# Performance work log

Measured on AMD Instinct MI355X. Metric: run time of the kernel, lower is better.

Reference implementation:

```python
import jax, jax.numpy as jnp
import numpy as np
from jax import lax

D_MODEL = 64      # feature_dim
D_STATE = 16      # state_dim
D_CONV = 4        # conv_dim
EXPAND = 2
D_INNER = EXPAND * D_MODEL          # 128
DT_RANK = (D_MODEL + 15) // 16      # ceil(d_model/16) = 4, mamba default
IN_DIM = 64
LN_EPS = 1e-3                        # keras LayerNormalization default epsilon


def setup_inputs() -> dict:
    key = jax.random.key(0)
    ks = jax.random.split(key, 12)
    B, L = 16, 8192
    s = 0.02
    x = jax.random.normal(ks[0], (B, L, IN_DIM), jnp.float32)
    W_in = jax.random.normal(ks[1], (IN_DIM, D_MODEL), jnp.float32) * s
    b_in = jnp.zeros((D_MODEL,), jnp.float32)
    in_proj_w = jax.random.normal(ks[2], (D_MODEL, 2 * D_INNER), jnp.float32) * s
    conv_w = jax.random.normal(ks[3], (D_INNER, D_CONV), jnp.float32) * 0.1
    conv_b = jnp.zeros((D_INNER,), jnp.float32)
    x_proj_w = jax.random.normal(ks[4], (D_INNER, DT_RANK + 2 * D_STATE), jnp.float32) * s
    dt_proj_w = jax.random.normal(ks[5], (DT_RANK, D_INNER), jnp.float32) * (DT_RANK ** -0.5)
    # dt bias init so softplus(dt) lands roughly in [dt_min, dt_max]
    dt = jnp.exp(jax.random.uniform(ks[6], (D_INNER,)) * (np.log(0.1) - np.log(0.001)) + np.log(0.001))
    dt_proj_b = dt + jnp.log(-jnp.expm1(-dt))  # inverse softplus
    A_log = jnp.log(jnp.broadcast_to(jnp.arange(1, D_STATE + 1, dtype=jnp.float32), (D_INNER, D_STATE)))
    D_skip = jnp.ones((D_INNER,), jnp.float32)
    out_proj_w = jax.random.normal(ks[7], (D_INNER, D_MODEL), jnp.float32) * s
    ln_gamma = jnp.ones((D_MODEL,), jnp.float32)
    ln_beta = jnp.zeros((D_MODEL,), jnp.float32)
    return {"x": x, "W_in": W_in, "b_in": b_in, "in_proj_w": in_proj_w,
            "conv_w": conv_w, "conv_b": conv_b, "x_proj_w": x_proj_w,
            "dt_proj_w": dt_proj_w, "dt_proj_b": dt_proj_b, "A_log": A_log,
            "D_skip": D_skip, "out_proj_w": out_proj_w,
            "ln_gamma": ln_gamma, "ln_beta": ln_beta}


def reference(x, W_in, b_in, in_proj_w, conv_w, conv_b, x_proj_w,
              dt_proj_w, dt_proj_b, A_log, D_skip, out_proj_w, ln_gamma, ln_beta):
    B, L, _ = x.shape
    # Conv1D kernel_size=1 input projection
    xin = x @ W_in + b_in                          # [B,L,D_MODEL]
    # --- Mamba ---
    xz = xin @ in_proj_w                           # [B,L,2*D_INNER]
    xc, z = xz[..., :D_INNER], xz[..., D_INNER:]
    # causal depthwise conv (groups=d_inner, padding=d_conv-1, crop to L)
    xp = jnp.pad(xc, ((0, 0), (D_CONV - 1, 0), (0, 0)))
    xconv = conv_b
    for k in range(D_CONV):
        xconv = xconv + xp[:, k:k + L, :] * conv_w[:, k]
    u = jax.nn.silu(xconv)                         # [B,L,D_INNER]
    dbc = u @ x_proj_w                             # [B,L,DT_RANK+2*D_STATE]
    dt = jax.nn.softplus(dbc[..., :DT_RANK] @ dt_proj_w + dt_proj_b)   # [B,L,D_INNER]
    Bm = dbc[..., DT_RANK:DT_RANK + D_STATE]       # [B,L,D_STATE]
    Cm = dbc[..., DT_RANK + D_STATE:]              # [B,L,D_STATE]
    A = -jnp.exp(A_log)                            # [D_INNER,D_STATE]

    def step(h, xs):
        dt_t, b_t, c_t, u_t = xs                   # [B,Di],[B,Ds],[B,Ds],[B,Di]
        dA = jnp.exp(dt_t[:, :, None] * A)         # [B,Di,Ds]
        h = dA * h + (dt_t * u_t)[:, :, None] * b_t[:, None, :]
        y = jnp.einsum('bds,bs->bd', h, c_t)
        return h, y

    xs = (jnp.swapaxes(dt, 0, 1), jnp.swapaxes(Bm, 0, 1),
          jnp.swapaxes(Cm, 0, 1), jnp.swapaxes(u, 0, 1))
    h0 = jnp.zeros((B, D_INNER, D_STATE), x.dtype)
    _, ys = lax.scan(step, h0, xs)                 # ys: [L,B,D_INNER]
    y = jnp.swapaxes(ys, 0, 1) + u * D_skip
    y = y * jax.nn.silu(z)
    h_out = y @ out_proj_w                         # [B,L,D_MODEL]
    # residual + LayerNorm
    res = h_out + xin
    mu = jnp.mean(res, axis=-1, keepdims=True)
    var = jnp.mean(jnp.square(res - mu), axis=-1, keepdims=True)
    return ln_gamma * (res - mu) * lax.rsqrt(var + LN_EPS) + ln_beta
```

## Files before the change

### kernel.cpp

```cpp
#include <hip/hip_runtime.h>
#include <hip/hip_bf16.h>
#include <hip/hip_fp16.h>

#define B_SZ   16
#define L_SZ   8192
#define DM     64
#define DI     128
#define NCH    256
#define CLEN   32
#define CH     64
#define RT     80
#define PA     72
#define PU     136
#define PC     132
#define LN_EPS 1e-3f

typedef float  f4 __attribute__((ext_vector_type(4)));
typedef short  s8 __attribute__((ext_vector_type(8)));
typedef unsigned short u16;
typedef unsigned int   u32;
#define MFMA16 __builtin_amdgcn_mfma_f32_16x16x32_bf16

__device__ __forceinline__ u16 f2bfu(float f) {
    u32 u = __float_as_uint(f);
    return (u16)((u + 0x7FFFu + ((u >> 16) & 1u)) >> 16);
}
__device__ __forceinline__ u32 pk2bf(float a, float b) {
    return (u32)f2bfu(a) | ((u32)f2bfu(b) << 16);
}
__device__ __forceinline__ float bflo(u32 u) { return __uint_as_float(u << 16); }
__device__ __forceinline__ float bfhi(u32 u) { return __uint_as_float(u & 0xFFFF0000u); }
__device__ __forceinline__ float bfu2f(u16 h) { return __uint_as_float((u32)h << 16); }
__device__ __forceinline__ float h2f(u32 lo16) {
    return __half2float(__ushort_as_half((u16)(lo16 & 0xFFFFu)));
}
__device__ __forceinline__ float fsig(float v) {
    return __builtin_amdgcn_rcpf(1.f + __expf(-v));
}
__device__ __forceinline__ float fsp(float v) {
    return fmaxf(v, 0.f) + __logf(1.f + __expf(-fabsf(v)));
}

__global__ __launch_bounds__(256) void k_prep(
    const float* __restrict__ W_in, const float* __restrict__ in_proj,
    const float* __restrict__ x_proj, const float* __restrict__ Wout,
    u16* __restrict__ Wf1, u16* __restrict__ Wf2,
    u16* __restrict__ Wf3, u16* __restrict__ Wf4)
{
    const int tid = threadIdx.x;
    for (int g = tid; g < 512; g += 256) {
        int lane = g & 63, ks = (g >> 6) & 1, nt = g >> 7;
        int n = nt * 16 + (lane & 15), kb = ks * 32 + (lane >> 4) * 8;
        for (int j = 0; j < 8; j++) Wf1[g * 8 + j] = f2bfu(W_in[(kb + j) * 64 + n]);
    }
    for (int g = tid; g < 2048; g += 256) {
        int lane = g & 63, ks = (g >> 6) & 1, nt = g >> 7;
        int n = nt * 16 + (lane & 15), kb = ks * 32 + (lane >> 4) * 8;
        for (int j = 0; j < 8; j++) Wf2[g * 8 + j] = f2bfu(in_proj[(kb + j) * 256 + n]);
    }
    for (int g = tid; g < 768; g += 256) {
        int lane = g & 63, ks = (g >> 6) & 3, nt = g >> 8;
        int n = nt * 16 + (lane & 15), kb = ks * 32 + (lane >> 4) * 8;
        for (int j = 0; j < 8; j++)
            Wf3[g * 8 + j] = f2bfu(n < 36 ? x_proj[(kb + j) * 36 + n] : 0.f);
    }
    for (int g = tid; g < 1024; g += 256) {
        int lane = g & 63, ks = (g >> 6) & 3, nt = g >> 8;
        int n = nt * 16 + (lane & 15), kb = ks * 32 + (lane >> 4) * 8;
        for (int j = 0; j < 8; j++) Wf4[g * 8 + j] = f2bfu(Wout[(kb + j) * 64 + n]);
    }
}

__global__ __launch_bounds__(256, 4) void k_frontend(
    const float* __restrict__ x, const float* __restrict__ b_in,
    const float* __restrict__ conv_w, const float* __restrict__ conv_b,
    const float* __restrict__ dt_w, const float* __restrict__ dt_b,
    const u16* __restrict__ Wf1, const u16* __restrict__ Wf2, const u16* __restrict__ Wf3,
    const float* __restrict__ A_log,
    float* __restrict__ xin_g, u32* __restrict__ dtu_g,
    float* __restrict__ B_g, float* __restrict__ C_g, u16* __restrict__ sz_g,
    float* __restrict__ hl_ws, float* __restrict__ sdt_ws)
{
    __shared__ __align__(16) char sm[40736];
    u16*   smA   = (u16*)sm;
    u16*   smB   = (u16*)(sm + 11520);
    u16*   smU   = (u16*)sm;
    float* smDtr = (float*)(sm + 17408);
    float* smBf  = (float*)(sm + 18432);
    u16*   smC   = (u16*)(sm + 23040);
    u32*   smDt  = (u32*)(sm + 23040);

    const int tid = threadIdx.x;
    const int w = tid >> 6, lane = tid & 63;
    const int n16 = lane & 15, quad = lane >> 4;
    const int b = blockIdx.y, c0 = blockIdx.x * CH;
    const long long tokbase = (long long)b * L_SZ + c0;

    for (int idx = tid; idx < RT * 16; idx += 256) {
        int r = idx >> 4, c4 = idx & 15;
        int l = c0 - 3 + r;
        float4 v = make_float4(0.f, 0.f, 0.f, 0.f);
        if (r < 67 && l >= 0)
            v = *(const float4*)(x + ((long long)b * L_SZ + l) * 64 + c4 * 4);
        *(uint2*)((char*)smA + r * 144 + c4 * 8) = make_uint2(pk2bf(v.x, v.y), pk2bf(v.z, v.w));
    }
    __syncthreads();

    {
        s8 b0 = *(const s8*)(Wf1 + ((w * 2 + 0) * 64 + lane) * 8);
        s8 b1 = *(const s8*)(Wf1 + ((w * 2 + 1) * 64 + lane) * 8);
        float bias = b_in[w * 16 + n16];
        for (int m = 0; m < 5; m++) {
            int ar = m * 16 + n16;
            s8 a0 = *(const s8*)(smA + ar * PA + quad * 8);
            s8 a1 = *(const s8*)(smA + ar * PA + 32 + quad * 8);
            f4 acc = {0.f, 0.f, 0.f, 0.f};
            acc = MFMA16(a0, b0, acc, 0, 0, 0);
            acc = MFMA16(a1, b1, acc, 0, 0, 0);
#pragma unroll
            for (int reg = 0; reg < 4; reg++) {
                int rr = m * 16 + quad * 4 + reg;
                float v = acc[reg] + bias;
                smB[rr * PA + w * 16 + n16] = f2bfu(v);
                if (rr >= 3 && rr < 67)
                    xin_g[(tokbase + rr - 3) * 64 + w * 16 + n16] = v;
            }
        }
    }
    __syncthreads();

    {
        s8 bf[4][2];
#pragma unroll
        for (int i = 0; i < 4; i++)
#pragma unroll
            for (int ks = 0; ks < 2; ks++)
                bf[i][ks] = *(const s8*)(Wf2 + (((w * 4 + i) * 2 + ks) * 64 + lane) * 8);
        for (int m = 0; m < 5; m++) {
            int ar = m * 16 + n16;
            s8 a0 = *(const s8*)(smB + ar * PA + quad * 8);
            s8 a1 = *(const s8*)(smB + ar * PA + 32 + quad * 8);
#pragma unroll
            for (int i = 0; i < 4; i++) {
                f4 acc = {0.f, 0.f, 0.f, 0.f};
                acc = MFMA16(a0, bf[i][0], acc, 0, 0, 0);
                acc = MFMA16(a1, bf[i][1], acc, 0, 0, 0);
                int cg = (w * 4 + i) * 16 + n16;
#pragma unroll
                for (int reg = 0; reg < 4; reg++) {
                    int rr = m * 16 + quad * 4 + reg;
                    float v = acc[reg];
                    if (cg < 128) {
                        if (rr < 67) {
                            int l = c0 - 3 + rr;
                            smC[rr * PC + cg] = f2bfu(l >= 0 ? v : 0.f);
                        }
                    } else if (rr >= 3 && rr < 67) {
                        sz_g[(tokbase + rr - 3) * 128 + (cg - 128)] = f2bfu(v * fsig(v));
                    }
                }
            }
        }
    }
    __syncthreads();

    {
        const int d2 = lane * 2, ctb = w * 16;
        float4 cw0 = ((const float4*)conv_w)[d2];
        float4 cw1 = ((const float4*)conv_w)[d2 + 1];
        float cb0 = conv_b[d2], cb1 = conv_b[d2 + 1];
        u32 r0 = *(const u32*)((char*)smC + (ctb + 0) * 264 + lane * 4);
        u32 r1 = *(const u32*)((char*)smC + (ctb + 1) * 264 + lane * 4);
        u32 r2 = *(const u32*)((char*)smC + (ctb + 2) * 264 + lane * 4);
#pragma unroll 4
        for (int j = 0; j < 16; j++) {
            int ct = ctb + j;
            u32 r3 = *(const u32*)((char*)smC + (ct + 3) * 264 + lane * 4);
            float v0 = cb0 + bflo(r0) * cw0.x + bflo(r1) * cw0.y + bflo(r2) * cw0.z + bflo(r3) * cw0.w;
            float v1 = cb1 + bfhi(r0) * cw1.x + bfhi(r1) * cw1.y + bfhi(r2) * cw1.z + bfhi(r3) * cw1.w;
            u32 pk = pk2bf(v0 * fsig(v0), v1 * fsig(v1));
            *(u32*)(smU + ct * PU + d2) = pk;
            r0 = r1; r1 = r2; r2 = r3;
        }
    }
    __syncthreads();

    {
        s8 bf3[3][4];
#pragma unroll
        for (int nt = 0; nt < 3; nt++)
#pragma unroll
            for (int ks = 0; ks < 4; ks++)
                bf3[nt][ks] = *(const s8*)(Wf3 + ((nt * 4 + ks) * 64 + lane) * 8);
        f4 acc[3] = {{0.f,0.f,0.f,0.f},{0.f,0.f,0.f,0.f},{0.f,0.f,0.f,0.f}};
        int ar = w * 16 + n16;
#pragma unroll
        for (int ks = 0; ks < 4; ks++) {
            s8 a = *(const s8*)(smU + ar * PU + ks * 32 + quad * 8);
#pragma unroll
            for (int nt = 0; nt < 3; nt++) acc[nt] = MFMA16(a, bf3[nt][ks], acc[nt], 0, 0, 0);
        }
#pragma unroll
        for (int nt = 0; nt < 3; nt++) {
            int c = nt * 16 + n16;
#pragma unroll
            for (int reg = 0; reg < 4; reg++) {
                int rr = w * 16 + quad * 4 + reg;
                float v = acc[nt][reg];
                long long t = tokbase + rr;
                if (c < 4)       smDtr[rr * 4 + c] = v;
                else if (c < 20) { B_g[t * 16 + (c - 4)] = v; smBf[rr * 16 + (c - 4)] = v; }
                else if (c < 36) C_g[t * 16 + (c - 20)] = v;
            }
        }
    }
    __syncthreads();

    {
        const int o2 = lane * 2, grp = w;
        float w00 = dt_w[o2],       w01 = dt_w[o2 + 1];
        float w10 = dt_w[128 + o2], w11 = dt_w[128 + o2 + 1];
        float w20 = dt_w[256 + o2], w21 = dt_w[256 + o2 + 1];
        float w30 = dt_w[384 + o2], w31 = dt_w[384 + o2 + 1];
        float b0 = dt_b[o2], b1 = dt_b[o2 + 1];
#pragma unroll 4
        for (int j = 0; j < 16; j++) {
            int ct = grp * 16 + j;
            float4 q = *(const float4*)(smDtr + ct * 4);
            float v0 = b0 + q.x * w00 + q.y * w10 + q.z * w20 + q.w * w30;
            float v1 = b1 + q.x * w01 + q.y * w11 + q.z * w21 + q.w * w31;
            u32 hpk = (u32)__half_as_ushort(__float2half_rn(fsp(v0))) |
                      ((u32)__half_as_ushort(__float2half_rn(fsp(v1))) << 16);
            smDt[ct * 64 + lane] = hpk;
            u32 upk = *(const u32*)(smU + ct * PU + o2);
            u32 pk0 = (hpk & 0xFFFFu) | (upk << 16);
            u32 pk1 = (hpk >> 16) | (upk & 0xFFFF0000u);
            *(uint2*)(dtu_g + (tokbase + ct) * 128 + o2) = make_uint2(pk0, pk1);
        }
    }
    __syncthreads();

    {
        const int d = tid & 127, cs = tid >> 7;
        const int j2 = d >> 1, hi = d & 1;
        float A[16];
#pragma unroll
        for (int s = 0; s < 16; s++) A[s] = -__expf(A_log[d * 16 + s]);
        const float A0 = A[0];
        bool chain = true;
#pragma unroll
        for (int s = 1; s < 16; s++)
            chain = chain && (fabsf(A[s] - (float)(s + 1) * A0) <= 1e-4f * fabsf(A[s]));

        float h[16];
#pragma unroll
        for (int s = 0; s < 16; s++) h[s] = 0.f;
        float sdt = 0.f;

        if (chain) {
            for (int i = 0; i < CLEN; i++) {
                int t = cs * CLEN + i;
                u32 q = smDt[t * 64 + j2];
                float dtv = __half2float(__ushort_as_half((u16)(hi ? (q >> 16) : (q & 0xFFFFu))));
                float uv  = bfu2f(smU[t * PU + d]);
                float du  = dtv * uv;  sdt += dtv;
                float4 b0 = *(const float4*)(smBf + t * 16);
                float4 b1 = *(const float4*)(smBf + t * 16 + 4);
                float4 b2 = *(const float4*)(smBf + t * 16 + 8);
                float4 b3 = *(const float4*)(smBf + t * 16 + 12);
                float p = __expf(dtv * A0), dA = p;
                h[0] = dA * h[0] + du * b0.x;
                dA *= p; h[1]  = dA * h[1]  + du * b0.y;
                dA *= p; h[2]  = dA * h[2]  + du * b0.z;
                dA *= p; h[3]  = dA * h[3]  + du * b0.w;
                dA *= p; h[4]  = dA * h[4]  + du * b1.x;
                dA *= p; h[5]  = dA * h[5]  + du * b1.y;
                dA *= p; h[6]  = dA * h[6]  + du * b1.z;
                dA *= p; h[7]  = dA * h[7]  + du * b1.w;
                dA *= p; h[8]  = dA * h[8]  + du * b2.x;
                dA *= p; h[9]  = dA * h[9]  + du * b2.y;
                dA *= p; h[10] = dA * h[10] + du * b2.z;
                dA *= p; h[11] = dA * h[11] + du * b2.w;
                dA *= p; h[12] = dA * h[12] + du * b3.x;
                dA *= p; h[13] = dA * h[13] + du * b3.y;
                dA *= p; h[14] = dA * h[14] + du * b3.z;
                dA *= p; h[15] = dA * h[15] + du * b3.w;
            }
        } else {
            for (int i = 0; i < CLEN; i++) {
                int t = cs * CLEN + i;
                u32 q = smDt[t * 64 + j2];
                float dtv = __half2float(__ushort_as_half((u16)(hi ? (q >> 16) : (q & 0xFFFFu))));
                float uv  = bfu2f(smU[t * PU + d]);
                float du  = dtv * uv;  sdt += dtv;
                const float* Bp = smBf + t * 16;
#pragma unroll
                for (int s = 0; s < 16; s++) h[s] = __expf(dtv * A[s]) * h[s] + du * Bp[s];
            }
        }

        const int ch = blockIdx.x * 2 + cs;
        float4* hp4 = (float4*)(hl_ws + (((long long)b * NCH + ch) * 128 + d) * 16);
        hp4[0] = make_float4(h[0], h[1], h[2], h[3]);
        hp4[1] = make_float4(h[4], h[5], h[6], h[7]);
        hp4[2] = make_float4(h[8], h[9], h[10], h[11]);
        hp4[3] = make_float4(h[12], h[13], h[14], h[15]);
        sdt_ws[((long long)b * NCH + ch) * 128 + d] = sdt;
    }
}

__global__ __launch_bounds__(128) void k_combine(
    const float* __restrict__ A_log, float* __restrict__ hl_ws,
    const float* __restrict__ sdt_ws)
{
    int gid = blockIdx.x * 128 + threadIdx.x;
    int b = gid >> 11;
    int rem = gid & 2047;
    int d = rem >> 4;
    float A = -__expf(A_log[rem]);
    float h = 0.f;
    for (int c = 0; c < NCH; c++) {
        long long o = ((long long)b * NCH + c) * 2048 + rem;
        float v = hl_ws[o];
        float sdt = sdt_ws[((long long)b * NCH + c) * 128 + d];
        hl_ws[o] = h;
        h = __expf(A * sdt) * h + v;
    }
}

__global__ __launch_bounds__(256, 4) void k_backend(
    const u32* __restrict__ dtu_g, const float* __restrict__ B_g,
    const float* __restrict__ C_g, const u16* __restrict__ sz_g,
    const float* __restrict__ A_log, const float* __restrict__ D_skip,
    const float* __restrict__ hin_ws, const float* __restrict__ xin_g,
    const u16* __restrict__ Wf4, const float* __restrict__ gamma,
    const float* __restrict__ beta, float* __restrict__ out)
{
    __shared__ __align__(16) char sm[34048];
    u16*   sy   = (u16*)sm;
    float* smR  = (float*)(sm + 17408);

    const int tid = threadIdx.x;
    const int cb = blockIdx.x, b = blockIdx.y;
    const long long tok0 = (long long)b * L_SZ + (long long)cb * 64;

    {
        const int d = tid & 127, half = tid >> 7;
        float A[16];
#pragma unroll
        for (int s = 0; s < 16; s++) A[s] = -__expf(A_log[d * 16 + s]);
        const float A0 = A[0];
        bool chain = true;
#pragma unroll
        for (int s = 1; s < 16; s++)
            chain = chain && (fabsf(A[s] - (float)(s + 1) * A0) <= 1e-4f * fabsf(A[s]));

        float h[16];
        {
            const float4* hp = (const float4*)(hin_ws +
                (((long long)b * NCH + 2 * cb + half) * 128 + d) * 16);
            float4 h0 = hp[0], h1 = hp[1], h2 = hp[2], h3 = hp[3];
            h[0]=h0.x; h[1]=h0.y; h[2]=h0.z; h[3]=h0.w;
            h[4]=h1.x; h[5]=h1.y; h[6]=h1.z; h[7]=h1.w;
            h[8]=h2.x; h[9]=h2.y; h[10]=h2.z; h[11]=h2.w;
            h[12]=h3.x; h[13]=h3.y; h[14]=h3.z; h[15]=h3.w;
        }
        const float Dv = D_skip[d];

        if (chain) {
            for (int i = 0; i < CLEN; i++) {
                int t = half * CLEN + i;
                u32 pk = dtu_g[(tok0 + t) * 128 + d];
                float dtv = h2f(pk);
                float uv  = bfhi(pk);
                float du  = dtv * uv;
                const float4* Bp = (const float4*)(B_g + (tok0 + t) * 16);
                float4 b0 = Bp[0], b1 = Bp[1], b2 = Bp[2], b3 = Bp[3];
                const float4* Cp = (const float4*)(C_g + (tok0 + t) * 16);
                float4 c0 = Cp[0], c1 = Cp[1], c2 = Cp[2], c3 = Cp[3];
                float p = __expf(dtv * A0), dA = p;
                h[0] = dA * h[0] + du * b0.x; float ys = h[0] * c0.x;
                dA *= p; h[1]  = dA * h[1]  + du * b0.y; ys += h[1]  * c0.y;
                dA *= p; h[2]  = dA * h[2]  + du * b0.z; ys += h[2]  * c0.z;
                dA *= p; h[3]  = dA * h[3]  + du * b0.w; ys += h[3]  * c0.w;
                dA *= p; h[4]  = dA * h[4]  + du * b1.x; ys += h[4]  * c1.x;
                dA *= p; h[5]  = dA * h[5]  + du * b1.y; ys += h[5]  * c1.y;
                dA *= p; h[6]  = dA * h[6]  + du * b1.z; ys += h[6]  * c1.z;
                dA *= p; h[7]  = dA * h[7]  + du * b1.w; ys += h[7]  * c1.w;
                dA *= p; h[8]  = dA * h[8]  + du * b2.x; ys += h[8]  * c2.x;
                dA *= p; h[9]  = dA * h[9]  + du * b2.y; ys += h[9]  * c2.y;
                dA *= p; h[10] = dA * h[10] + du * b2.z; ys += h[10] * c2.z;
                dA *= p; h[11] = dA * h[11] + du * b2.w; ys += h[11] * c2.w;
                dA *= p; h[12] = dA * h[12] + du * b3.x; ys += h[12] * c3.x;
                dA *= p; h[13] = dA * h[13] + du * b3.y; ys += h[13] * c3.y;
                dA *= p; h[14] = dA * h[14] + du * b3.z; ys += h[14] * c3.z;
                dA *= p; h[15] = dA * h[15] + du * b3.w; ys += h[15] * c3.w;
                float szv = bfu2f(sz_g[(tok0 + t) * 128 + d]);
                sy[t * PU + d] = f2bfu((ys + uv * Dv) * szv);
            }
        } else {
            for (int i = 0; i < CLEN; i++) {
                int t = half * CLEN + i;
                u32 pk = dtu_g[(tok0 + t) * 128 + d];
                float dtv = h2f(pk);
                float uv  = bfhi(pk);
                float du  = dtv * uv;
                const float4* Bp = (const float4*)(B_g + (tok0 + t) * 16);
                float4 b0 = Bp[0], b1 = Bp[1], b2 = Bp[2], b3 = Bp[3];
                float Bv[16] = { b0.x, b0.y, b0.z, b0.w, b1.x, b1.y, b1.z, b1.w,
                                 b2.x, b2.y, b2.z, b2.w, b3.x, b3.y, b3.z, b3.w };
                const float4* Cp = (const float4*)(C_g + (tok0 + t) * 16);
                float4 c0 = Cp[0], c1 = Cp[1], c2 = Cp[2], c3 = Cp[3];
                float Cv[16] = { c0.x, c0.y, c0.z, c0.w, c1.x, c1.y, c1.z, c1.w,
                                 c2.x, c2.y, c2.z, c2.w, c3.x, c3.y, c3.z, c3.w };
                float ys = 0.f;
#pragma unroll
                for (int s = 0; s < 16; s++) {
                    h[s] = __expf(dtv * A[s]) * h[s] + du * Bv[s];
                    ys += h[s] * Cv[s];
                }
                float szv = bfu2f(sz_g[(tok0 + t) * 128 + d]);
                sy[t * PU + d] = f2bfu((ys + uv * Dv) * szv);
            }
        }
    }
    __syncthreads();

    const int w = tid >> 6, lane = tid & 63;
    const int n16 = lane & 15, quad = lane >> 4;
    {
        s8 bf[4];
#pragma unroll
        for (int ks = 0; ks < 4; ks++)
            bf[ks] = *(const s8*)(Wf4 + ((w * 4 + ks) * 64 + lane) * 8);
#pragma unroll
        for (int m = 0; m < 4; m++) {
            int ar = m * 16 + n16;
            f4 acc = {0.f, 0.f, 0.f, 0.f};
#pragma unroll
            for (int ks = 0; ks < 4; ks++) {
                s8 a = *(const s8*)(sy + ar * PU + ks * 32 + quad * 8);
                acc = MFMA16(a, bf[ks], acc, 0, 0, 0);
            }
#pragma unroll
            for (int reg = 0; reg < 4; reg++) {
                int rr = m * 16 + quad * 4 + reg;
                smR[rr * 65 + w * 16 + n16] = acc[reg];
            }
        }
    }
    __syncthreads();

    {
        int o = tid & 63, wv = tid >> 6;
        float g = gamma[o], bb = beta[o];
        for (int j = 0; j < 16; j++) {
            int rr = wv * 16 + j;
            float r = smR[rr * 65 + o] + xin_g[(tok0 + rr) * 64 + o];
            float s = r;
#pragma unroll
            for (int mS = 0; mS < 6; mS++) s += __shfl_xor(s, 1 << mS, 64);
            float mu = s * (1.f / 64.f);
            float dv = r - mu;
            float vs = dv * dv;
#pragma unroll
            for (int mS = 0; mS < 6; mS++) vs += __shfl_xor(vs, 1 << mS, 64);
            out[(tok0 + rr) * 64 + o] = g * dv * rsqrtf(vs * (1.f / 64.f) + LN_EPS) + bb;
        }
    }
}

extern "C" void kernel_launch(void* const* d_in, const int* in_sizes, int n_in,
                              void* d_out, int out_size, void* d_ws, size_t ws_size,
                              hipStream_t stream)
{
    const float* x       = (const float*)d_in[0];
    const float* W_in    = (const float*)d_in[1];
    const float* b_in    = (const float*)d_in[2];
    const float* in_proj = (const float*)d_in[3];
    const float* conv_w  = (const float*)d_in[4];
    const float* conv_b  = (const float*)d_in[5];
    const float* x_proj  = (const float*)d_in[6];
    const float* dt_w    = (const float*)d_in[7];
    const float* dt_b    = (const float*)d_in[8];
    const float* A_log   = (const float*)d_in[9];
    const float* D_skip  = (const float*)d_in[10];
    const float* Wout    = (const float*)d_in[11];
    const float* gamma   = (const float*)d_in[12];
    const float* beta    = (const float*)d_in[13];
    float* out = (float*)d_out;

    const long long NT = (long long)B_SZ * L_SZ;
    char* ws = (char*)d_ws;
    float*  xin_g = (float*)ws;   ws += NT * 64 * 4;
    u32*    dtu_g = (u32*)ws;     ws += NT * 128 * 4;
    float*  B_g   = (float*)ws;   ws += NT * 16 * 4;
    float*  C_g   = (float*)ws;   ws += NT * 16 * 4;
    u16*    sz_g  = (u16*)ws;     ws += NT * 128 * 2;
    float*  hl_ws  = (float*)ws;  ws += (long long)B_SZ * NCH * 2048 * 4;
    float*  sdt_ws = (float*)ws;  ws += (long long)B_SZ * NCH * 128 * 4;
    u16* Wf1 = (u16*)ws; ws += 4096 * 2;
    u16* Wf2 = (u16*)ws; ws += 16384 * 2;
    u16* Wf3 = (u16*)ws; ws += 6144 * 2;
    u16* Wf4 = (u16*)ws; ws += 8192 * 2;

    k_prep<<<1, 256, 0, stream>>>(W_in, in_proj, x_proj, Wout, Wf1, Wf2, Wf3, Wf4);

    k_frontend<<<dim3(L_SZ / CH, B_SZ), 256, 0, stream>>>(
        x, b_in, conv_w, conv_b, dt_w, dt_b, Wf1, Wf2, Wf3, A_log,
        xin_g, dtu_g, B_g, C_g, sz_g, hl_ws, sdt_ws);

    k_combine<<<256, 128, 0, stream>>>(A_log, hl_ws, sdt_ws);

    k_backend<<<dim3(L_SZ / 64, B_SZ), 256, 0, stream>>>(
        dtu_g, B_g, C_g, sz_g, A_log, D_skip, hl_ws, xin_g,
        Wf4, gamma, beta, out);
}
```

Measured before the change: 302.5 us.

## Break decay-power dependency chain and alias backend shared buffers for occupancy

Replaces the serial running product of decay factors (dA *= p) with powers built from p, p2, p4 and p8, which shortens the dependent multiply chain in both scan loops. In the backend kernel the MFMA output staging buffer now aliases the bf16 y tile. An extra barrier holds the accumulators in registers until all waves finish reading the tile. This halves LDS per block and raises launch bounds from 4 to 6 blocks per CU, trading one more sync and register pressure for occupancy.

```diff
diff --git a/kernel.cpp b/kernel.cpp
--- a/kernel.cpp
+++ b/kernel.cpp
@@ -268,23 +268,25 @@
                 float4 b1 = *(const float4*)(smBf + t * 16 + 4);
                 float4 b2 = *(const float4*)(smBf + t * 16 + 8);
                 float4 b3 = *(const float4*)(smBf + t * 16 + 12);
-                float p = __expf(dtv * A0), dA = p;
-                h[0] = dA * h[0] + du * b0.x;
-                dA *= p; h[1]  = dA * h[1]  + du * b0.y;
-                dA *= p; h[2]  = dA * h[2]  + du * b0.z;
-                dA *= p; h[3]  = dA * h[3]  + du * b0.w;
-                dA *= p; h[4]  = dA * h[4]  + du * b1.x;
-                dA *= p; h[5]  = dA * h[5]  + du * b1.y;
-                dA *= p; h[6]  = dA * h[6]  + du * b1.z;
-                dA *= p; h[7]  = dA * h[7]  + du * b1.w;
-                dA *= p; h[8]  = dA * h[8]  + du * b2.x;
-                dA *= p; h[9]  = dA * h[9]  + du * b2.y;
-                dA *= p; h[10] = dA * h[10] + du * b2.z;
-                dA *= p; h[11] = dA * h[11] + du * b2.w;
-                dA *= p; h[12] = dA * h[12] + du * b3.x;
-                dA *= p; h[13] = dA * h[13] + du * b3.y;
-                dA *= p; h[14] = dA * h[14] + du * b3.z;
-                dA *= p; h[15] = dA * h[15] + du * b3.w;
+                float p  = __expf(dtv * A0);
+                float p2 = p * p,  p3 = p2 * p,  p4 = p2 * p2;
+                float p8 = p4 * p4;
+                h[0]  = p        * h[0]  + du * b0.x;
+                h[1]  = p2       * h[1]  + du * b0.y;
+                h[2]  = p3       * h[2]  + du * b0.z;
+                h[3]  = p4       * h[3]  + du * b0.w;
+                h[4]  = (p4*p)   * h[4]  + du * b1.x;
+                h[5]  = (p4*p2)  * h[5]  + du * b1.y;
+                h[6]  = (p4*p3)  * h[6]  + du * b1.z;
+                h[7]  = p8       * h[7]  + du * b1.w;
+                h[8]  = (p8*p)   * h[8]  + du * b2.x;
+                h[9]  = (p8*p2)  * h[9]  + du * b2.y;
+                h[10] = (p8*p3)  * h[10] + du * b2.z;
+                h[11] = (p8*p4)  * h[11] + du * b2.w;
+                h[12] = (p8*p4*p)  * h[12] + du * b3.x;
+                h[13] = (p8*p4*p2) * h[13] + du * b3.y;
+                h[14] = (p8*p4*p3) * h[14] + du * b3.z;
+                h[15] = (p8*p8)    * h[15] + du * b3.w;
             }
         } else {
             for (int i = 0; i < CLEN; i++) {
@@ -328,7 +330,7 @@
     }
 }
 
-__global__ __launch_bounds__(256, 4) void k_backend(
+__global__ __launch_bounds__(256, 6) void k_backend(
     const u32* __restrict__ dtu_g, const float* __restrict__ B_g,
     const float* __restrict__ C_g, const u16* __restrict__ sz_g,
     const float* __restrict__ A_log, const float* __restrict__ D_skip,
@@ -336,9 +338,9 @@
     const u16* __restrict__ Wf4, const float* __restrict__ gamma,
     const float* __restrict__ beta, float* __restrict__ out)
 {
-    __shared__ __align__(16) char sm[34048];
+    __shared__ __align__(16) char sm[17408];
     u16*   sy   = (u16*)sm;
-    float* smR  = (float*)(sm + 17408);
+    float* smR  = (float*)sm;
 
     const int tid = threadIdx.x;
     const int cb = blockIdx.x, b = blockIdx.y;
@@ -378,23 +380,25 @@
                 float4 b0 = Bp[0], b1 = Bp[1], b2 = Bp[2], b3 = Bp[3];
                 const float4* Cp = (const float4*)(C_g + (tok0 + t) * 16);
                 float4 c0 = Cp[0], c1 = Cp[1], c2 = Cp[2], c3 = Cp[3];
-                float p = __expf(dtv * A0), dA = p;
-                h[0] = dA * h[0] + du * b0.x; float ys = h[0] * c0.x;
-                dA *= p; h[1]  = dA * h[1]  + du * b0.y; ys += h[1]  * c0.y;
-                dA *= p; h[2]  = dA * h[2]  + du * b0.z; ys += h[2]  * c0.z;
-                dA *= p; h[3]  = dA * h[3]  + du * b0.w; ys += h[3]  * c0.w;
-                dA *= p; h[4]  = dA * h[4]  + du * b1.x; ys += h[4]  * c1.x;
-                dA *= p; h[5]  = dA * h[5]  + du * b1.y; ys += h[5]  * c1.y;
-                dA *= p; h[6]  = dA * h[6]  + du * b1.z; ys += h[6]  * c1.z;
-                dA *= p; h[7]  = dA * h[7]  + du * b1.w; ys += h[7]  * c1.w;
-                dA *= p; h[8]  = dA * h[8]  + du * b2.x; ys += h[8]  * c2.x;
-                dA *= p; h[9]  = dA * h[9]  + du * b2.y; ys += h[9]  * c2.y;
-                dA *= p; h[10] = dA * h[10] + du * b2.z; ys += h[10] * c2.z;
-                dA *= p; h[11] = dA * h[11] + du * b2.w; ys += h[11] * c2.w;
-                dA *= p; h[12] = dA * h[12] + du * b3.x; ys += h[12] * c3.x;
-                dA *= p; h[13] = dA * h[13] + du * b3.y; ys += h[13] * c3.y;
-                dA *= p; h[14] = dA * h[14] + du * b3.z; ys += h[14] * c3.z;
-                dA *= p; h[15] = dA * h[15] + du * b3.w; ys += h[15] * c3.w;
+                float p  = __expf(dtv * A0);
+                float p2 = p * p,  p3 = p2 * p,  p4 = p2 * p2;
+                float p8 = p4 * p4;
+                h[0]  = p        * h[0]  + du * b0.x; float ys = h[0] * c0.x;
+                h[1]  = p2       * h[1]  + du * b0.y; ys += h[1]  * c0.y;
+                h[2]  = p3       * h[2]  + du * b0.z; ys += h[2]  * c0.z;
+                h[3]  = p4       * h[3]  + du * b0.w; ys += h[3]  * c0.w;
+                h[4]  = (p4*p)   * h[4]  + du * b1.x; ys += h[4]  * c1.x;
+                h[5]  = (p4*p2)  * h[5]  + du * b1.y; ys += h[5]  * c1.y;
+                h[6]  = (p4*p3)  * h[6]  + du * b1.z; ys += h[6]  * c1.z;
+                h[7]  = p8       * h[7]  + du * b1.w; ys += h[7]  * c1.w;
+                h[8]  = (p8*p)   * h[8]  + du * b2.x; ys += h[8]  * c2.x;
+                h[9]  = (p8*p2)  * h[9]  + du * b2.y; ys += h[9]  * c2.y;
+                h[10] = (p8*p3)  * h[10] + du * b2.z; ys += h[10] * c2.z;
+                h[11] = (p8*p4)  * h[11] + du * b2.w; ys += h[11] * c2.w;
+                h[12] = (p8*p4*p)  * h[12] + du * b3.x; ys += h[12] * c3.x;
+                h[13] = (p8*p4*p2) * h[13] + du * b3.y; ys += h[13] * c3.y;
+                h[14] = (p8*p4*p3) * h[14] + du * b3.z; ys += h[14] * c3.z;
+                h[15] = (p8*p8)    * h[15] + du * b3.w; ys += h[15] * c3.w;
                 float szv = bfu2f(sz_g[(tok0 + t) * 128 + d]);
                 sy[t * PU + d] = f2bfu((ys + uv * Dv) * szv);
             }
@@ -428,6 +432,7 @@
 
     const int w = tid >> 6, lane = tid & 63;
     const int n16 = lane & 15, quad = lane >> 4;
+    f4 accm[4];
     {
         s8 bf[4];
 #pragma unroll
@@ -442,12 +447,19 @@
                 s8 a = *(const s8*)(sy + ar * PU + ks * 32 + quad * 8);
                 acc = MFMA16(a, bf[ks], acc, 0, 0, 0);
             }
+            accm[m] = acc;
+        }
+    }
+    __syncthreads();
+
+    {
+#pragma unroll
+        for (int m = 0; m < 4; m++)
 #pragma unroll
             for (int reg = 0; reg < 4; reg++) {
                 int rr = m * 16 + quad * 4 + reg;
-                smR[rr * 65 + w * 16 + n16] = acc[reg];
-            }
-        }
+                smR[rr * 65 + w * 16 + n16] = accm[m][reg];
+            }
     }
     __syncthreads();
 
```

After: 296.0 us. -2.2%, faster.
